# Optimization experiments

Hardware: AMD Instinct MI355X
Metric: run time of the kernel (lower is better)

Reference implementation:

```python
import jax, jax.numpy as jnp
import numpy as np
import math

DIM = 1024
HEADS = 16
DIM_HEAD = 64
INNER = HEADS * DIM_HEAD
NUM_BUCKETS = 32
MAX_DISTANCE = 128


def setup_inputs() -> dict:
    key = jax.random.key(0)
    ks = jax.random.split(key, 6)
    x = jax.random.normal(ks[0], (2, 2048, DIM), dtype=jnp.float32)
    Wq = jax.random.normal(ks[1], (DIM, INNER), dtype=jnp.float32) * (DIM ** -0.5)
    Wkv = jax.random.normal(ks[2], (DIM, 2 * DIM_HEAD), dtype=jnp.float32) * (DIM ** -0.5)
    Wout = jax.random.normal(ks[3], (INNER, DIM), dtype=jnp.float32) * (INNER ** -0.5)
    bout = jnp.zeros((DIM,), dtype=jnp.float32)
    rel_emb = jax.random.normal(ks[4], (NUM_BUCKETS, HEADS), dtype=jnp.float32) * 0.02
    return {"x": x, "Wq": Wq, "Wkv": Wkv, "Wout": Wout, "bout": bout, "rel_emb": rel_emb}


def _relative_position_bucket(rel_pos, num_buckets=NUM_BUCKETS, max_distance=MAX_DISTANCE):
    # rel_pos: [i, j] int32, k_pos - q_pos
    n = jnp.maximum(-rel_pos, 0)
    max_exact = num_buckets // 2
    is_small = n < max_exact
    n_safe = jnp.maximum(n, 1)  # avoid log(0); masked by is_small anyway
    val_if_large = max_exact + (
        jnp.log(n_safe.astype(jnp.float32) / max_exact)
        / math.log(max_distance / max_exact)
        * (num_buckets - max_exact)
    ).astype(jnp.int32)
    val_if_large = jnp.minimum(val_if_large, num_buckets - 1)
    return jnp.where(is_small, n, val_if_large)


def reference(x, Wq, Wkv, Wout, bout, rel_emb):
    b, n, _ = x.shape
    scale = DIM_HEAD ** -0.5
    bias_scale = DIM_HEAD ** 0.5

    q = (x @ Wq).reshape(b, n, HEADS, DIM_HEAD).transpose(0, 2, 1, 3) * scale  # [b,h,n,d]
    kv = x @ Wkv  # [b,n,2d]
    k, v = kv[..., :DIM_HEAD], kv[..., DIM_HEAD:]  # shared single-head K/V [b,n,d]

    sim = jnp.einsum('bhid,bjd->bhij', q, k)

    # T5 relative position bias
    pos = jnp.arange(n, dtype=jnp.int32)
    rel_pos = pos[None, :] - pos[:, None]  # [i,j] = k_pos - q_pos
    rp_bucket = _relative_position_bucket(rel_pos)
    bias = rel_emb[rp_bucket]  # [i,j,h]
    sim = sim + jnp.transpose(bias, (2, 0, 1))[None] * bias_scale

    # causal mask: mask strictly-upper triangle
    causal_mask = jnp.triu(jnp.ones((n, n), dtype=bool), k=1)
    neg = jnp.finfo(sim.dtype).max
    sim = jnp.where(causal_mask[None, None], -neg, sim)

    attn = jax.nn.softmax(sim, axis=-1)
    out = jnp.einsum('bhij,bjd->bhid', attn, v)
    out = out.transpose(0, 2, 1, 3).reshape(b, n, INNER)
    return out @ Wout + bout
```

## Files before the change

kernel.cpp:

```cpp
#include <hip/hip_runtime.h>
#include <cstdint>
#include <cmath>

typedef _Float16 half8 __attribute__((ext_vector_type(8)));
typedef unsigned short ushort8 __attribute__((ext_vector_type(8)));
typedef float floatx4 __attribute__((ext_vector_type(4)));

#define VT_STRIDE 2080

__device__ __forceinline__ unsigned short f2h(float f) {
    union { _Float16 h; unsigned short u; } cv;
    cv.h = (_Float16)f;
    return cv.u;
}

__device__ __forceinline__ void gld_lds16(const unsigned short* g, unsigned short* l) {
    __builtin_amdgcn_global_load_lds(
        (const __attribute__((address_space(1))) unsigned int*)g,
        (__attribute__((address_space(3))) unsigned int*)l, 16, 0, 0);
}

__global__ void cast_x_kernel(const float* __restrict__ x, unsigned short* __restrict__ xh, int n8) {
    int idx = blockIdx.x * blockDim.x + threadIdx.x;
    if (idx >= n8) return;
    const float4* p = (const float4*)x;
    float4 a = p[idx * 2], b = p[idx * 2 + 1];
    ushort8 o;
    o[0] = f2h(a.x); o[1] = f2h(a.y); o[2] = f2h(a.z); o[3] = f2h(a.w);
    o[4] = f2h(b.x); o[5] = f2h(b.y); o[6] = f2h(b.z); o[7] = f2h(b.w);
    *(ushort8*)(xh + (size_t)idx * 8) = o;
}

__global__ void transpose_fused_kernel(const float* __restrict__ Wq, const float* __restrict__ Wkv,
                                       const float* __restrict__ Wout,
                                       unsigned short* __restrict__ Wqkvt, unsigned short* __restrict__ Wot) {
    __shared__ float tile[32][33];
    int bxi = blockIdx.x;
    const float* in; unsigned short* out; int C; int cb;
    if (bxi < 32)      { in = Wq;   out = Wqkvt;                 C = 1024; cb = bxi; }
    else if (bxi < 36) { in = Wkv;  out = Wqkvt + 1024 * 1024;   C = 128;  cb = bxi - 32; }
    else               { in = Wout; out = Wot;                   C = 1024; cb = bxi - 36; }
    int bx = cb * 32, by = blockIdx.y * 32;
    int x = threadIdx.x, y0 = threadIdx.y;
    #pragma unroll
    for (int k = 0; k < 4; k++) {
        int y = y0 + k * 8;
        tile[y][x] = in[(size_t)(by + y) * C + bx + x];
    }
    __syncthreads();
    #pragma unroll
    for (int k = 0; k < 4; k++) {
        int y = y0 + k * 8;
        out[(size_t)(bx + y) * 1024 + by + x] = f2h(tile[x][y]);
    }
}

template<int MODE>
__global__ __launch_bounds__(256) void gemm_mn(
    const unsigned short* __restrict__ A, const unsigned short* __restrict__ Bt,
    unsigned short* __restrict__ oq, unsigned short* __restrict__ ok,
    unsigned short* __restrict__ ov, float* __restrict__ of,
    const float* __restrict__ bias)
{
    __shared__ __align__(16) unsigned short As[2][128 * 64];
    __shared__ __align__(16) unsigned short Bs[2][128 * 64];
    const int K = 1024;
    int t = threadIdx.x;
    int w = t >> 6, lane = t & 63, g = lane >> 4, il = lane & 15;
    int wr = w >> 1, wc = w & 1;
    int m0 = blockIdx.y * 128, n0 = blockIdx.x * 128;

    int l8 = lane >> 3, b8 = lane & 7;
    int swz = (b8 ^ l8) * 8;
    const unsigned short* Ag = A  + (size_t)(m0 + w * 32 + l8) * K + swz;
    const unsigned short* Bg = Bt + (size_t)(n0 + w * 32 + l8) * K + swz;
    int e0 = (g ^ (il & 7)) * 8;

    floatx4 acc[4][4] = {};

    #pragma unroll
    for (int q = 0; q < 4; q++) {
        gld_lds16(Ag + (size_t)(q * 8) * K, &As[0][(w * 32 + q * 8) * 64]);
        gld_lds16(Bg + (size_t)(q * 8) * K, &Bs[0][(w * 32 + q * 8) * 64]);
    }

    int cb = 0;
    for (int k0 = 0; k0 < K; k0 += 64, cb ^= 1) {
        __syncthreads();
        if (k0 + 64 < K) {
            #pragma unroll
            for (int q = 0; q < 4; q++) {
                gld_lds16(Ag + (size_t)(q * 8) * K + k0 + 64, &As[cb ^ 1][(w * 32 + q * 8) * 64]);
                gld_lds16(Bg + (size_t)(q * 8) * K + k0 + 64, &Bs[cb ^ 1][(w * 32 + q * 8) * 64]);
            }
        }
        const unsigned short* Ac = &As[cb][0];
        const unsigned short* Bc = &Bs[cb][0];
        #pragma unroll
        for (int ks = 0; ks < 2; ks++) {
            half8 a[4];
            #pragma unroll
            for (int mt = 0; mt < 4; mt++)
                a[mt] = *(const half8*)&Ac[(wr * 64 + mt * 16 + il) * 64 + (e0 ^ (ks * 32))];
            #pragma unroll
            for (int nt = 0; nt < 4; nt++) {
                half8 b = *(const half8*)&Bc[(wc * 64 + nt * 16 + il) * 64 + (e0 ^ (ks * 32))];
                #pragma unroll
                for (int mt = 0; mt < 4; mt++)
                    acc[mt][nt] = __builtin_amdgcn_mfma_f32_16x16x32_f16(a[mt], b, acc[mt][nt], 0, 0, 0);
            }
        }
    }

    #pragma unroll
    for (int mt = 0; mt < 4; mt++) {
        #pragma unroll
        for (int nt = 0; nt < 4; nt++) {
            #pragma unroll
            for (int r = 0; r < 4; r++) {
                int row = m0 + wr * 64 + mt * 16 + 4 * g + r;
                int col = n0 + wc * 64 + nt * 16 + il;
                float v = acc[mt][nt][r];
                if (MODE == 0) {
                    if (col < 1024) {
                        int b = row >> 11, i = row & 2047, h = col >> 6, d = col & 63;
                        oq[(size_t)((b * 16 + h) * 2048 + i) * 64 + d] = f2h(v * 0.18033688011112042f);
                    } else if (col < 1088) {
                        ok[(size_t)row * 64 + (col - 1024)] = f2h(v);
                    } else {
                        int b = row >> 11, j = row & 2047;
                        ov[(size_t)((b << 6) + (col - 1088)) * VT_STRIDE + j] = f2h(v);
                    }
                } else {
                    of[(size_t)row * 1024 + col] = v + bias[col];
                }
            }
        }
    }
}

__global__ __launch_bounds__(256) void attn_kernel(
    const unsigned short* __restrict__ qh, const unsigned short* __restrict__ kh,
    const unsigned short* __restrict__ vt, const float* __restrict__ rel_emb,
    unsigned short* __restrict__ ob)
{
    __shared__ float bias_tab[256];
    __shared__ __align__(16) unsigned short Ks[2][64 * 64];
    __shared__ __align__(16) unsigned short Vs[64 * 64];
    __shared__ __align__(16) unsigned short Pl[64 * 72];

    int bx = 31 - blockIdx.y;
    int bh = blockIdx.x;
    int b = bh >> 4, h = bh & 15;
    int t = threadIdx.x;
    int w = t >> 6, lane = t & 63, g = lane >> 4, il = lane & 15;

    {
        int dlt = t;
        int bucket;
        if (dlt < 16) bucket = dlt;
        else {
            float lg = logf((float)dlt * 0.0625f) / 2.0794415416798357f;
            int vv = 16 + (int)(lg * 16.0f);
            bucket = vv < 31 ? vv : 31;
        }
        bias_tab[dlt] = rel_emb[bucket * 16 + h] * 11.541560327111708f;
    }
    float cb31 = rel_emb[31 * 16 + h] * 11.541560327111708f;

    const unsigned short* kbase = kh + (size_t)b * (2048 * 64);
    const unsigned short* vbase = vt + (size_t)b * (64 * VT_STRIDE);
    int prow = (w * 16 + il) * 72;

    int l8 = lane >> 3, b8 = lane & 7;
    int swz = (b8 ^ l8) * 8;
    const unsigned short* kg_base = kbase + (size_t)(w * 16 + l8) * 64 + swz;
    const unsigned short* vg_base = vbase + (size_t)(w * 16 + l8) * VT_STRIDE + swz;
    int e0 = (g ^ (il & 7)) * 8;

    int iw = bx * 64 + w * 16;
    int i_glob = iw + il;
    const unsigned short* qrow = qh + (size_t)(bh * 2048 + i_glob) * 64;
    half8 qf0 = *(const half8*)(qrow + g * 8);
    half8 qf1 = *(const half8*)(qrow + 32 + g * 8);
    floatx4 O[4] = {};
    float m_run = -1e30f, l_run = 0.0f;

    gld_lds16(kg_base,                 &Ks[0][(w * 16) * 64]);
    gld_lds16(kg_base + 8 * 64,        &Ks[0][(w * 16 + 8) * 64]);
    gld_lds16(vg_base,                 &Vs[(w * 16) * 64]);
    gld_lds16(vg_base + 8 * VT_STRIDE, &Vs[(w * 16 + 8) * 64]);

    for (int c = 0; c <= bx; c++) {
        __syncthreads();
        if (c < bx) {
            const unsigned short* kg = kg_base + (size_t)(c + 1) * 4096;
            unsigned short* kd = &Ks[(c + 1) & 1][0];
            gld_lds16(kg,          &kd[(w * 16) * 64]);
            gld_lds16(kg + 8 * 64, &kd[(w * 16 + 8) * 64]);
        }
        const unsigned short* Kc = &Ks[c & 1][0];
        int j0 = c * 64;

        floatx4 S[4] = {};
        #pragma unroll
        for (int jt = 0; jt < 4; jt++) {
            half8 k0 = *(const half8*)&Kc[jt * 1024 + il * 64 + e0];
            half8 k1 = *(const half8*)&Kc[jt * 1024 + il * 64 + (e0 ^ 32)];
            S[jt] = __builtin_amdgcn_mfma_f32_16x16x32_f16(k0, qf0, S[jt], 0, 0, 0);
            S[jt] = __builtin_amdgcn_mfma_f32_16x16x32_f16(k1, qf1, S[jt], 0, 0, 0);
        }
        half8 vf[8];
        #pragma unroll
        for (int ks = 0; ks < 2; ks++)
            #pragma unroll
            for (int dt = 0; dt < 4; dt++)
                vf[ks * 4 + dt] = *(const half8*)&Vs[dt * 1024 + il * 64 + (e0 ^ (ks * 32))];

        asm volatile("s_waitcnt lgkmcnt(0)" ::: "memory");
        __builtin_amdgcn_s_barrier();
        if (c < bx) {
            const unsigned short* vg = vg_base + (c + 1) * 64;
            gld_lds16(vg,                 &Vs[(w * 16) * 64]);
            gld_lds16(vg + 8 * VT_STRIDE, &Vs[(w * 16 + 8) * 64]);
        }

        float s[16];
        if (c + 3 <= bx) {
            #pragma unroll
            for (int q2 = 0; q2 < 16; q2++) s[q2] = S[q2 >> 2][q2 & 3] + cb31;
        } else if (c < bx) {
            #pragma unroll
            for (int jt = 0; jt < 4; jt++)
                #pragma unroll
                for (int r = 0; r < 4; r++)
                    s[jt * 4 + r] = S[jt][r] + bias_tab[i_glob - (j0 + jt * 16 + 4 * g + r)];
        } else {
            #pragma unroll
            for (int jt = 0; jt < 4; jt++) {
                #pragma unroll
                for (int r = 0; r < 4; r++) {
                    int delta = i_glob - (j0 + jt * 16 + 4 * g + r);
                    int di = delta > 0 ? delta : 0;
                    s[jt * 4 + r] = (delta >= 0) ? (S[jt][r] + bias_tab[di]) : -1e30f;
                }
            }
        }
        float m8[8];
        #pragma unroll
        for (int q2 = 0; q2 < 8; q2++) m8[q2] = fmaxf(s[q2], s[q2 + 8]);
        #pragma unroll
        for (int q2 = 0; q2 < 4; q2++) m8[q2] = fmaxf(m8[q2], m8[q2 + 4]);
        float mx = fmaxf(fmaxf(m8[0], m8[1]), fmaxf(m8[2], m8[3]));
        mx = fmaxf(mx, __shfl_xor(mx, 16));
        mx = fmaxf(mx, __shfl_xor(mx, 32));
        float m_new = fmaxf(m_run, mx);
        float alpha = __builtin_amdgcn_exp2f(m_run - m_new);
        float p[16];
        #pragma unroll
        for (int q2 = 0; q2 < 16; q2++) p[q2] = __builtin_amdgcn_exp2f(s[q2] - m_new);
        float ps[8];
        #pragma unroll
        for (int q2 = 0; q2 < 8; q2++) ps[q2] = p[q2] + p[q2 + 8];
        #pragma unroll
        for (int q2 = 0; q2 < 4; q2++) ps[q2] += ps[q2 + 4];
        float psum = (ps[0] + ps[1]) + (ps[2] + ps[3]);
        psum += __shfl_xor(psum, 16);
        psum += __shfl_xor(psum, 32);
        l_run = l_run * alpha + psum;
        m_run = m_new;
        float arow[4];
        #pragma unroll
        for (int r = 0; r < 4; r++) arow[r] = __shfl(alpha, 4 * g + r);
        #pragma unroll
        for (int dt = 0; dt < 4; dt++)
            #pragma unroll
            for (int r = 0; r < 4; r++) O[dt][r] *= arow[r];
        #pragma unroll
        for (int jt = 0; jt < 4; jt++) {
            uint2 u;
            u.x = (unsigned int)f2h(p[jt * 4 + 0]) | ((unsigned int)f2h(p[jt * 4 + 1]) << 16);
            u.y = (unsigned int)f2h(p[jt * 4 + 2]) | ((unsigned int)f2h(p[jt * 4 + 3]) << 16);
            *(uint2*)&Pl[prow + jt * 16 + 4 * g] = u;
        }
        #pragma unroll
        for (int ks = 0; ks < 2; ks++) {
            half8 pf = *(const half8*)&Pl[prow + ks * 32 + g * 8];
            #pragma unroll
            for (int dt = 0; dt < 4; dt++)
                O[dt] = __builtin_amdgcn_mfma_f32_16x16x32_f16(pf, vf[ks * 4 + dt], O[dt], 0, 0, 0);
        }
    }
    float inv[4];
    #pragma unroll
    for (int r = 0; r < 4; r++) inv[r] = 1.0f / __shfl(l_run, 4 * g + r);
    #pragma unroll
    for (int dt = 0; dt < 4; dt++) {
        #pragma unroll
        for (int r = 0; r < 4; r++) {
            int i = iw + 4 * g + r;
            int d = dt * 16 + il;
            ob[(size_t)(b * 2048 + i) * 1024 + h * 64 + d] = f2h(O[dt][r] * inv[r]);
        }
    }
}

extern "C" void kernel_launch(void* const* d_in, const int* in_sizes, int n_in,
                              void* d_out, int out_size, void* d_ws, size_t ws_size,
                              hipStream_t stream) {
    const float* x    = (const float*)d_in[0];
    const float* Wq   = (const float*)d_in[1];
    const float* Wkv  = (const float*)d_in[2];
    const float* Wout = (const float*)d_in[3];
    const float* bout = (const float*)d_in[4];
    const float* rel  = (const float*)d_in[5];
    float* out = (float*)d_out;

    unsigned short* ws    = (unsigned short*)d_ws;
    unsigned short* xh    = ws;
    unsigned short* qh    = xh + 4194304;
    unsigned short* kh    = qh + 4194304;
    unsigned short* vt    = kh + 262144;
    unsigned short* Wqkvt = vt + 2 * 64 * VT_STRIDE;
    unsigned short* Wot   = Wqkvt + 1179648;
    unsigned short* ob    = xh;

    cast_x_kernel<<<2048, 256, 0, stream>>>(x, xh, 524288);
    transpose_fused_kernel<<<dim3(68, 32), dim3(32, 8), 0, stream>>>(Wq, Wkv, Wout, Wqkvt, Wot);
    gemm_mn<0><<<dim3(9, 32), 256, 0, stream>>>(xh, Wqkvt, qh, kh, vt, nullptr, nullptr);
    attn_kernel<<<dim3(32, 32), 256, 0, stream>>>(qh, kh, vt, rel, ob);
    gemm_mn<2><<<dim3(8, 32), 256, 0, stream>>>(ob, Wot, nullptr, nullptr, nullptr, out, bout);
}
```

Measured before the change: 175.1 us.

## Pair causal attention query tiles per block and tighten GEMM pipeline barriers

The attention kernel now has each block process two query tiles, one long (31-pr) and one short (pr), so every block does the same total causal work. The grid is halved and the K/V prefetch carries over from the first tile into the second. The softmax rescale is skipped when no row maximum increases, and the constant far-distance bias is folded out, since a per-row constant cancels in softmax. The GEMMs swap grid axes so adjacent blocks share the B tile, and replace __syncthreads with explicit vmcnt/lgkmcnt waits plus barriers, aiming to overlap loads with MFMA better at the cost of fewer attention blocks for occupancy.

Measured after the change: 178.2 us. No clear change (+1.8%).

```diff
diff --git a/kernel.cpp b/kernel.cpp
--- a/kernel.cpp
+++ b/kernel.cpp
@@ -68,7 +68,7 @@
     int t = threadIdx.x;
     int w = t >> 6, lane = t & 63, g = lane >> 4, il = lane & 15;
     int wr = w >> 1, wc = w & 1;
-    int m0 = blockIdx.y * 128, n0 = blockIdx.x * 128;
+    int m0 = blockIdx.x * 128, n0 = blockIdx.y * 128;
 
     int l8 = lane >> 3, b8 = lane & 7;
     int swz = (b8 ^ l8) * 8;
@@ -86,14 +86,19 @@
 
     int cb = 0;
     for (int k0 = 0; k0 < K; k0 += 64, cb ^= 1) {
-        __syncthreads();
         if (k0 + 64 < K) {
             #pragma unroll
             for (int q = 0; q < 4; q++) {
                 gld_lds16(Ag + (size_t)(q * 8) * K + k0 + 64, &As[cb ^ 1][(w * 32 + q * 8) * 64]);
                 gld_lds16(Bg + (size_t)(q * 8) * K + k0 + 64, &Bs[cb ^ 1][(w * 32 + q * 8) * 64]);
             }
-        }
+            asm volatile("s_waitcnt vmcnt(8)" ::: "memory");
+        } else {
+            asm volatile("s_waitcnt vmcnt(0)" ::: "memory");
+        }
+        __builtin_amdgcn_s_barrier();
+        __builtin_amdgcn_sched_barrier(0);
+
         const unsigned short* Ac = &As[cb][0];
         const unsigned short* Bc = &Bs[cb][0];
         #pragma unroll
@@ -110,6 +115,8 @@
                     acc[mt][nt] = __builtin_amdgcn_mfma_f32_16x16x32_f16(a[mt], b, acc[mt][nt], 0, 0, 0);
             }
         }
+        asm volatile("s_waitcnt lgkmcnt(0)" ::: "memory");
+        __builtin_amdgcn_s_barrier();
     }
 
     #pragma unroll
@@ -149,12 +156,13 @@
     __shared__ __align__(16) unsigned short Vs[64 * 64];
     __shared__ __align__(16) unsigned short Pl[64 * 72];
 
-    int bx = 31 - blockIdx.y;
+    int pr = blockIdx.y;
     int bh = blockIdx.x;
     int b = bh >> 4, h = bh & 15;
     int t = threadIdx.x;
     int w = t >> 6, lane = t & 63, g = lane >> 4, il = lane & 15;
 
+    float cbv = rel_emb[31 * 16 + h];
     {
         int dlt = t;
         int bucket;
@@ -164,9 +172,8 @@
             int vv = 16 + (int)(lg * 16.0f);
             bucket = vv < 31 ? vv : 31;
         }
-        bias_tab[dlt] = rel_emb[bucket * 16 + h] * 11.541560327111708f;
-    }
-    float cb31 = rel_emb[31 * 16 + h] * 11.541560327111708f;
+        bias_tab[dlt] = (rel_emb[bucket * 16 + h] - cbv) * 11.541560327111708f;
+    }
 
     const unsigned short* kbase = kh + (size_t)b * (2048 * 64);
     const unsigned short* vbase = vt + (size_t)b * (64 * VT_STRIDE);
@@ -178,129 +185,143 @@
     const unsigned short* vg_base = vbase + (size_t)(w * 16 + l8) * VT_STRIDE + swz;
     int e0 = (g ^ (il & 7)) * 8;
 
-    int iw = bx * 64 + w * 16;
-    int i_glob = iw + il;
-    const unsigned short* qrow = qh + (size_t)(bh * 2048 + i_glob) * 64;
-    half8 qf0 = *(const half8*)(qrow + g * 8);
-    half8 qf1 = *(const half8*)(qrow + 32 + g * 8);
-    floatx4 O[4] = {};
-    float m_run = -1e30f, l_run = 0.0f;
+    int kb = 0;
 
     gld_lds16(kg_base,                 &Ks[0][(w * 16) * 64]);
     gld_lds16(kg_base + 8 * 64,        &Ks[0][(w * 16 + 8) * 64]);
     gld_lds16(vg_base,                 &Vs[(w * 16) * 64]);
     gld_lds16(vg_base + 8 * VT_STRIDE, &Vs[(w * 16 + 8) * 64]);
 
-    for (int c = 0; c <= bx; c++) {
-        __syncthreads();
-        if (c < bx) {
-            const unsigned short* kg = kg_base + (size_t)(c + 1) * 4096;
-            unsigned short* kd = &Ks[(c + 1) & 1][0];
-            gld_lds16(kg,          &kd[(w * 16) * 64]);
-            gld_lds16(kg + 8 * 64, &kd[(w * 16 + 8) * 64]);
-        }
-        const unsigned short* Kc = &Ks[c & 1][0];
-        int j0 = c * 64;
-
-        floatx4 S[4] = {};
+    for (int tt = 0; tt < 2; tt++) {
+        int bx = tt ? pr : (31 - pr);
+        int iw = bx * 64 + w * 16;
+        int i_glob = iw + il;
+        const unsigned short* qrow = qh + (size_t)(bh * 2048 + i_glob) * 64;
+        half8 qf0 = *(const half8*)(qrow + g * 8);
+        half8 qf1 = *(const half8*)(qrow + 32 + g * 8);
+        floatx4 O[4] = {};
+        float m_run = -1e30f, l_run = 0.0f;
+
+        for (int c = 0; c <= bx; c++) {
+            __syncthreads();
+            bool pre  = (c < bx);
+            bool preT = (!pre) && (tt == 0);
+            if (pre || preT) {
+                int nc = pre ? c + 1 : 0;
+                const unsigned short* kg = kg_base + (size_t)nc * 4096;
+                unsigned short* kd = &Ks[kb ^ 1][0];
+                gld_lds16(kg,          &kd[(w * 16) * 64]);
+                gld_lds16(kg + 8 * 64, &kd[(w * 16 + 8) * 64]);
+            }
+            const unsigned short* Kc = &Ks[kb][0];
+            int j0 = c * 64;
+
+            floatx4 S[4] = {};
+            #pragma unroll
+            for (int jt = 0; jt < 4; jt++) {
+                half8 k0 = *(const half8*)&Kc[jt * 1024 + il * 64 + e0];
+                half8 k1 = *(const half8*)&Kc[jt * 1024 + il * 64 + (e0 ^ 32)];
+                S[jt] = __builtin_amdgcn_mfma_f32_16x16x32_f16(k0, qf0, S[jt], 0, 0, 0);
+                S[jt] = __builtin_amdgcn_mfma_f32_16x16x32_f16(k1, qf1, S[jt], 0, 0, 0);
+            }
+            half8 vf[8];
+            #pragma unroll
+            for (int ks = 0; ks < 2; ks++)
+                #pragma unroll
+                for (int dt = 0; dt < 4; dt++)
+                    vf[ks * 4 + dt] = *(const half8*)&Vs[dt * 1024 + il * 64 + (e0 ^ (ks * 32))];
+
+            asm volatile("s_waitcnt lgkmcnt(0)" ::: "memory");
+            __builtin_amdgcn_s_barrier();
+            if (pre || preT) {
+                int nc = pre ? c + 1 : 0;
+                const unsigned short* vg = vg_base + nc * 64;
+                gld_lds16(vg,                 &Vs[(w * 16) * 64]);
+                gld_lds16(vg + 8 * VT_STRIDE, &Vs[(w * 16 + 8) * 64]);
+            }
+
+            float s[16];
+            if (c + 3 <= bx) {
+                #pragma unroll
+                for (int q2 = 0; q2 < 16; q2++) s[q2] = S[q2 >> 2][q2 & 3];
+            } else if (c < bx) {
+                #pragma unroll
+                for (int jt = 0; jt < 4; jt++)
+                    #pragma unroll
+                    for (int r = 0; r < 4; r++)
+                        s[jt * 4 + r] = S[jt][r] + bias_tab[i_glob - (j0 + jt * 16 + 4 * g + r)];
+            } else {
+                #pragma unroll
+                for (int jt = 0; jt < 4; jt++) {
+                    #pragma unroll
+                    for (int r = 0; r < 4; r++) {
+                        int delta = i_glob - (j0 + jt * 16 + 4 * g + r);
+                        int di = delta > 0 ? delta : 0;
+                        s[jt * 4 + r] = (delta >= 0) ? (S[jt][r] + bias_tab[di]) : -1e30f;
+                    }
+                }
+            }
+            float m8[8];
+            #pragma unroll
+            for (int q2 = 0; q2 < 8; q2++) m8[q2] = fmaxf(s[q2], s[q2 + 8]);
+            #pragma unroll
+            for (int q2 = 0; q2 < 4; q2++) m8[q2] = fmaxf(m8[q2], m8[q2 + 4]);
+            float mx = fmaxf(fmaxf(m8[0], m8[1]), fmaxf(m8[2], m8[3]));
+            mx = fmaxf(mx, __shfl_xor(mx, 16));
+            mx = fmaxf(mx, __shfl_xor(mx, 32));
+            if (__any(mx > m_run)) {
+                float m_new = fmaxf(m_run, mx);
+                float alpha = __builtin_amdgcn_exp2f(m_run - m_new);
+                l_run *= alpha;
+                float arow[4];
+                #pragma unroll
+                for (int r = 0; r < 4; r++) arow[r] = __shfl(alpha, 4 * g + r);
+                #pragma unroll
+                for (int dt = 0; dt < 4; dt++)
+                    #pragma unroll
+                    for (int r = 0; r < 4; r++) O[dt][r] *= arow[r];
+                m_run = m_new;
+            }
+            float p[16];
+            #pragma unroll
+            for (int q2 = 0; q2 < 16; q2++) p[q2] = __builtin_amdgcn_exp2f(s[q2] - m_run);
+            float ps[8];
+            #pragma unroll
+            for (int q2 = 0; q2 < 8; q2++) ps[q2] = p[q2] + p[q2 + 8];
+            #pragma unroll
+            for (int q2 = 0; q2 < 4; q2++) ps[q2] += ps[q2 + 4];
+            float psum = (ps[0] + ps[1]) + (ps[2] + ps[3]);
+            psum += __shfl_xor(psum, 16);
+            psum += __shfl_xor(psum, 32);
+            l_run += psum;
+
+            #pragma unroll
+            for (int jt = 0; jt < 4; jt++) {
+                uint2 u;
+                u.x = (unsigned int)f2h(p[jt * 4 + 0]) | ((unsigned int)f2h(p[jt * 4 + 1]) << 16);
+                u.y = (unsigned int)f2h(p[jt * 4 + 2]) | ((unsigned int)f2h(p[jt * 4 + 3]) << 16);
+                *(uint2*)&Pl[prow + jt * 16 + 4 * g] = u;
+            }
+            #pragma unroll
+            for (int ks = 0; ks < 2; ks++) {
+                half8 pf = *(const half8*)&Pl[prow + ks * 32 + g * 8];
+                #pragma unroll
+                for (int dt = 0; dt < 4; dt++)
+                    O[dt] = __builtin_amdgcn_mfma_f32_16x16x32_f16(pf, vf[ks * 4 + dt], O[dt], 0, 0, 0);
+            }
+            kb ^= 1;
+        }
+        float inv[4];
         #pragma unroll
-        for (int jt = 0; jt < 4; jt++) {
-            half8 k0 = *(const half8*)&Kc[jt * 1024 + il * 64 + e0];
-            half8 k1 = *(const half8*)&Kc[jt * 1024 + il * 64 + (e0 ^ 32)];
-            S[jt] = __builtin_amdgcn_mfma_f32_16x16x32_f16(k0, qf0, S[jt], 0, 0, 0);
-            S[jt] = __builtin_amdgcn_mfma_f32_16x16x32_f16(k1, qf1, S[jt], 0, 0, 0);
-        }
-        half8 vf[8];
+        for (int r = 0; r < 4; r++) inv[r] = 1.0f / __shfl(l_run, 4 * g + r);
         #pragma unroll
-        for (int ks = 0; ks < 2; ks++)
-            #pragma unroll
-            for (int dt = 0; dt < 4; dt++)
-                vf[ks * 4 + dt] = *(const half8*)&Vs[dt * 1024 + il * 64 + (e0 ^ (ks * 32))];
-
-        asm volatile("s_waitcnt lgkmcnt(0)" ::: "memory");
-        __builtin_amdgcn_s_barrier();
-        if (c < bx) {
-            const unsigned short* vg = vg_base + (c + 1) * 64;
-            gld_lds16(vg,                 &Vs[(w * 16) * 64]);
-            gld_lds16(vg + 8 * VT_STRIDE, &Vs[(w * 16 + 8) * 64]);
-        }
-
-        float s[16];
-        if (c + 3 <= bx) {
-            #pragma unroll
-            for (int q2 = 0; q2 < 16; q2++) s[q2] = S[q2 >> 2][q2 & 3] + cb31;
-        } else if (c < bx) {
-            #pragma unroll
-            for (int jt = 0; jt < 4; jt++)
-                #pragma unroll
-                for (int r = 0; r < 4; r++)
-                    s[jt * 4 + r] = S[jt][r] + bias_tab[i_glob - (j0 + jt * 16 + 4 * g + r)];
-        } else {
-            #pragma unroll
-            for (int jt = 0; jt < 4; jt++) {
-                #pragma unroll
-                for (int r = 0; r < 4; r++) {
-                    int delta = i_glob - (j0 + jt * 16 + 4 * g + r);
-                    int di = delta > 0 ? delta : 0;
-                    s[jt * 4 + r] = (delta >= 0) ? (S[jt][r] + bias_tab[di]) : -1e30f;
-                }
-            }
-        }
-        float m8[8];
-        #pragma unroll
-        for (int q2 = 0; q2 < 8; q2++) m8[q2] = fmaxf(s[q2], s[q2 + 8]);
-        #pragma unroll
-        for (int q2 = 0; q2 < 4; q2++) m8[q2] = fmaxf(m8[q2], m8[q2 + 4]);
-        float mx = fmaxf(fmaxf(m8[0], m8[1]), fmaxf(m8[2], m8[3]));
-        mx = fmaxf(mx, __shfl_xor(mx, 16));
-        mx = fmaxf(mx, __shfl_xor(mx, 32));
-        float m_new = fmaxf(m_run, mx);
-        float alpha = __builtin_amdgcn_exp2f(m_run - m_new);
-        float p[16];
-        #pragma unroll
-        for (int q2 = 0; q2 < 16; q2++) p[q2] = __builtin_amdgcn_exp2f(s[q2] - m_new);
-        float ps[8];
-        #pragma unroll
-        for (int q2 = 0; q2 < 8; q2++) ps[q2] = p[q2] + p[q2 + 8];
-        #pragma unroll
-        for (int q2 = 0; q2 < 4; q2++) ps[q2] += ps[q2 + 4];
-        float psum = (ps[0] + ps[1]) + (ps[2] + ps[3]);
-        psum += __shfl_xor(psum, 16);
-        psum += __shfl_xor(psum, 32);
-        l_run = l_run * alpha + psum;
-        m_run = m_new;
-        float arow[4];
-        #pragma unroll
-        for (int r = 0; r < 4; r++) arow[r] = __shfl(alpha, 4 * g + r);
-        #pragma unroll
-        for (int dt = 0; dt < 4; dt++)
-            #pragma unroll
-            for (int r = 0; r < 4; r++) O[dt][r] *= arow[r];
-        #pragma unroll
-        for (int jt = 0; jt < 4; jt++) {
-            uint2 u;
-            u.x = (unsigned int)f2h(p[jt * 4 + 0]) | ((unsigned int)f2h(p[jt * 4 + 1]) << 16);
-            u.y = (unsigned int)f2h(p[jt * 4 + 2]) | ((unsigned int)f2h(p[jt * 4 + 3]) << 16);
-            *(uint2*)&Pl[prow + jt * 16 + 4 * g] = u;
-        }
-        #pragma unroll
-        for (int ks = 0; ks < 2; ks++) {
-            half8 pf = *(const half8*)&Pl[prow + ks * 32 + g * 8];
-            #pragma unroll
-            for (int dt = 0; dt < 4; dt++)
-                O[dt] = __builtin_amdgcn_mfma_f32_16x16x32_f16(pf, vf[ks * 4 + dt], O[dt], 0, 0, 0);
-        }
-    }
-    float inv[4];
-    #pragma unroll
-    for (int r = 0; r < 4; r++) inv[r] = 1.0f / __shfl(l_run, 4 * g + r);
-    #pragma unroll
-    for (int dt = 0; dt < 4; dt++) {
-        #pragma unroll
-        for (int r = 0; r < 4; r++) {
-            int i = iw + 4 * g + r;
-            int d = dt * 16 + il;
-            ob[(size_t)(b * 2048 + i) * 1024 + h * 64 + d] = f2h(O[dt][r] * inv[r]);
+        for (int dt = 0; dt < 4; dt++) {
+            #pragma unroll
+            for (int r = 0; r < 4; r++) {
+                int i = iw + 4 * g + r;
+                int d = dt * 16 + il;
+                ob[(size_t)(b * 2048 + i) * 1024 + h * 64 + d] = f2h(O[dt][r] * inv[r]);
+            }
         }
     }
 }
@@ -327,7 +348,7 @@
 
     cast_x_kernel<<<2048, 256, 0, stream>>>(x, xh, 524288);
     transpose_fused_kernel<<<dim3(68, 32), dim3(32, 8), 0, stream>>>(Wq, Wkv, Wout, Wqkvt, Wot);
-    gemm_mn<0><<<dim3(9, 32), 256, 0, stream>>>(xh, Wqkvt, qh, kh, vt, nullptr, nullptr);
-    attn_kernel<<<dim3(32, 32), 256, 0, stream>>>(qh, kh, vt, rel, ob);
-    gemm_mn<2><<<dim3(8, 32), 256, 0, stream>>>(ob, Wot, nullptr, nullptr, nullptr, out, bout);
-}
+    gemm_mn<0><<<dim3(32, 9), 256, 0, stream>>>(xh, Wqkvt, qh, kh, vt, nullptr, nullptr);
+    attn_kernel<<<dim3(32, 16), 256, 0, stream>>>(qh, kh, vt, rel, ob);
+    gemm_mn<2><<<dim3(32, 8), 256, 0, stream>>>(ob, Wot, nullptr, nullptr, nullptr, out, bout);
+}
```
